# Performance work log

Measured on AMD Instinct MI355X. Metric: run time of the kernel, lower is better.

The kernel has to match this reference:

```python
import jax, jax.numpy as jnp
import numpy as np

B, L, EMB, H, NL, E, MAXA, PAD = 64, 512, 400, 256, 3, 512, 32, 0


def setup_inputs() -> dict:
    key = jax.random.key(0)
    ks = jax.random.split(key, 12)
    s = lambda k, shape: jax.random.normal(k, shape, jnp.float32) * 0.02
    Semb = jax.random.normal(ks[0], (B, EMB, L), jnp.float32)
    word_ids = jax.random.randint(ks[1], (B, L), 0, 30000)
    y1 = jax.random.randint(ks[2], (B,), 0, L - MAXA)
    span = jax.random.randint(ks[3], (B,), 0, MAXA)
    y2 = y1 + span
    edges = jax.random.randint(ks[4], (B, E, 2), 0, L)
    return dict(
        Semb=Semb,
        ans_sent_word_ids=word_ids,
        y1_in_sent=y1,
        y2_in_sent=y2,
        edges=edges,
        W1=s(ks[5], (H, EMB)),                 # Initialized_Conv1d (k=1, no bias)
        hw_lin_W=s(ks[6], (2, H, H)), hw_lin_b=jnp.zeros((2, H), jnp.float32),
        hw_gate_W=s(ks[7], (2, H, H)), hw_gate_b=jnp.zeros((2, H), jnp.float32),
        gcn_W=s(ks[8], (NL, H, H)), gcn_b=jnp.zeros((NL, H), jnp.float32),
        conv_W=s(ks[9], (1, NL * H)), conv_b=jnp.zeros((1,), jnp.float32),
        lin_W=s(ks[10], (L, L)), lin_b=jnp.zeros((L,), jnp.float32),
    )


def reference(Semb, ans_sent_word_ids, y1_in_sent, y2_in_sent, edges,
              W1, hw_lin_W, hw_lin_b, hw_gate_W, hw_gate_b,
              gcn_W, gcn_b, conv_W, conv_b, lin_W, lin_b):
    # 1x1 conv: [B, EMB, L] -> [B, H, L]
    x = jnp.einsum('oi,bit->bot', W1, Semb)
    # 2-layer Highway (dropout is identity in eval)
    for i in range(2):
        gate = jax.nn.sigmoid(jnp.einsum('oi,bit->bot', hw_gate_W[i], x) + hw_gate_b[i][None, :, None])
        nonlin = jnp.einsum('oi,bit->bot', hw_lin_W[i], x) + hw_lin_b[i][None, :, None]
        x = gate * nonlin + (1.0 - gate) * x
    maskS = (ans_sent_word_ids != PAD).astype(x.dtype)            # [B, L]
    # answer-span mask (Aemb itself is dead code in the original forward's output)
    pos = y1_in_sent[:, None] + jnp.arange(MAXA)                   # [B, MAXA]
    maskA = (pos <= y2_in_sent[:, None]).astype(x.dtype)
    # dense adjacency from edge list (undirected since gcn_directed=False)
    bidx = jnp.broadcast_to(jnp.arange(B)[:, None], (B, E))
    adj = jnp.zeros((B, L, L), x.dtype)
    adj = adj.at[bidx, edges[..., 0], edges[..., 1]].set(1.0)
    adj = adj.at[bidx, edges[..., 1], edges[..., 0]].set(1.0)
    # GCN (C-GCN style: W(Ax) + W(x), note bias counted twice, /(deg+1), relu)
    h = x.transpose(0, 2, 1)                                       # [B, L, H]
    denom = jnp.sum(adj, axis=2, keepdims=True) + 1.0              # [B, L, 1]
    outs = []
    for l in range(NL):
        Ax = jnp.einsum('bls,bsh->blh', adj, h)
        AxW = jnp.einsum('blh,oh->blo', Ax + h, gcn_W[l]) + 2.0 * gcn_b[l]
        h = jax.nn.relu(AxW / denom)
        outs.append(h)
    cat = jnp.concatenate(outs, axis=2)                            # [B, L, NL*H]
    y = jax.nn.relu(jnp.einsum('blc,oc->bol', cat, conv_W) + conv_b[None, :, None])  # [B,1,L]
    logits = (jnp.einsum('bol,ml->bom', y, lin_W) + lin_b).squeeze(1)                # [B,L]
    logits = logits * maskS + (1.0 - maskS) * (-1e30)
    return (logits, maskA)
```

## Files before the change

kernel.cpp:

```cpp
#include <hip/hip_runtime.h>
#include <cstdint>

#define B 64
#define L 512
#define EMB 400
#define KPAD 416
#define H 256
#define NL 3
#define NE 512
#define MAXA 32
#define M_TOT (B * L)

typedef unsigned short u16;
typedef float f32x4 __attribute__((ext_vector_type(4)));
typedef short short8 __attribute__((ext_vector_type(8)));
typedef u16 u16x8 __attribute__((ext_vector_type(8)));

__device__ __forceinline__ float b2f(u16 u) {
  unsigned v = ((unsigned)u) << 16;
  return __builtin_bit_cast(float, v);
}
__device__ __forceinline__ u16 f2b(float f) {
  unsigned u = __builtin_bit_cast(unsigned, f);
  unsigned r = (u + 0x7fffu + ((u >> 16) & 1u)) >> 16;
  return (u16)r;
}

#define GL16(g, l)                                                              \
  __builtin_amdgcn_global_load_lds((const __attribute__((address_space(1))) void*)(g), \
                                   (__attribute__((address_space(3))) void*)(l), 16, 0, 0)

__global__ __launch_bounds__(256, 2) void k_convT(const float* __restrict__ Semb,
                                                  const u16* __restrict__ W1b,
                                                  u16* __restrict__ Out) {
  __shared__ u16 smem[64 * KPAD + 256 * 32];
  __shared__ u16 tmp2[64][72];
  u16* At = smem;
  u16* Bt = smem + 64 * KPAD;

  const int t = threadIdx.x;
  const int wid = t >> 6, lane = t & 63;
  const int m0 = blockIdx.x * 64;
  const int b = m0 >> 9, l0 = m0 & 511;
  const int fr = lane & 15, kg = lane >> 4;
  const int r4 = t >> 2, ksg = t & 3;

  {
    const int kc0 = ksg * 8;
#pragma unroll
    for (int c = 0; c < 4; ++c)
      GL16(W1b + (size_t)(c * 64 + r4) * KPAD + kc0, Bt + (size_t)(c * 256 + wid * 64) * 8);
  }

  for (int et = 0; et < 7; ++et) {
    const int e0 = et * 64;
    const int erows = (et < 6) ? 64 : 32;
    {
      const int er = t >> 2, ls = (t & 3) * 16;
      if (er < erows) {
        if (e0 + er < EMB) {
          const float* src = Semb + ((size_t)b * EMB + e0 + er) * L + l0 + ls;
#pragma unroll
          for (int i = 0; i < 4; ++i) {
            const float4 v = *(const float4*)(src + i * 4);
            tmp2[er][ls + i * 4 + 0] = f2b(v.x);
            tmp2[er][ls + i * 4 + 1] = f2b(v.y);
            tmp2[er][ls + i * 4 + 2] = f2b(v.z);
            tmp2[er][ls + i * 4 + 3] = f2b(v.w);
          }
        } else {
#pragma unroll
          for (int i = 0; i < 16; ++i) tmp2[er][ls + i] = 0;
        }
      }
    }
    __syncthreads();
    {
      const int lr = t >> 2, es = (t & 3) * 16;
      if (es < erows) {
        u16x8 v0, v1;
#pragma unroll
        for (int i = 0; i < 8; ++i) v0[i] = tmp2[es + i][lr];
#pragma unroll
        for (int i = 0; i < 8; ++i) v1[i] = tmp2[es + 8 + i][lr];
        const int k = e0 + es;
        u16* dst = At + (((size_t)(k >> 5) * 64 + lr) * 4 + ((k & 31) >> 3)) * 8;
        *(u16x8*)dst = v0;
        *(u16x8*)(dst + 8) = v1;
      }
    }
    __syncthreads();
  }

  f32x4 acc[4][4] = {};
  for (int kk = 0; kk < (KPAD >> 5); ++kk) {
    if (kk > 0) {
      const int kc = kk * 32 + ksg * 8;
#pragma unroll
      for (int c = 0; c < 4; ++c)
        GL16(W1b + (size_t)(c * 64 + r4) * KPAD + kc, Bt + (size_t)(c * 256 + wid * 64) * 8);
    }
    asm volatile("s_waitcnt vmcnt(0)" ::: "memory");
    __builtin_amdgcn_s_barrier();
    asm volatile("" ::: "memory");
    short8 af[4], bf[4];
#pragma unroll
    for (int i = 0; i < 4; ++i) {
      af[i] = *(const short8*)(At + ((size_t)(kk * 64 + i * 16 + fr) * 4 + kg) * 8);
      bf[i] = *(const short8*)(Bt + ((size_t)(wid * 64 + i * 16 + fr) * 4 + kg) * 8);
    }
#pragma unroll
    for (int mi = 0; mi < 4; ++mi)
#pragma unroll
      for (int ni = 0; ni < 4; ++ni)
        acc[mi][ni] = __builtin_amdgcn_mfma_f32_16x16x32_bf16(af[mi], bf[ni], acc[mi][ni], 0, 0, 0);
    __builtin_amdgcn_s_barrier();
    asm volatile("" ::: "memory");
  }

  const int r0 = kg * 4;
  const int c0 = wid * 64 + fr;
#pragma unroll
  for (int ni = 0; ni < 4; ++ni) {
    const int col = c0 + ni * 16;
#pragma unroll
    for (int mi = 0; mi < 4; ++mi)
#pragma unroll
      for (int rr = 0; rr < 4; ++rr)
        Out[(size_t)(m0 + mi * 16 + r0 + rr) * H + col] = f2b(acc[mi][ni][rr]);
  }
}

__global__ __launch_bounds__(256, 2) void gemm64hw(
    const u16* __restrict__ A, const u16* __restrict__ Bw, const u16* __restrict__ B2w,
    const float* __restrict__ bias1, const float* __restrict__ bias2,
    u16* __restrict__ Out) {
  __shared__ u16 Bl0[256 * 32];
  __shared__ u16 Bl1[256 * 32];
  __shared__ u16 Cl0[256 * 32];
  __shared__ u16 Cl1[256 * 32];
  __shared__ u16 Al0[64 * 32];
  __shared__ u16 Al1[64 * 32];

  const int t = threadIdx.x;
  const int wid = t >> 6, lane = t & 63;
  const int m0 = blockIdx.x * 64;
  const int fr = lane & 15, kg = lane >> 4;
  const int r4 = t >> 2, ksg = t & 3;

  f32x4 acc[4][4] = {};
  f32x4 acc2[4][4] = {};

  auto stage = [&](u16* Ab, u16* Bb, u16* Cb, int kk) {
    const int kc = kk * 32 + ksg * 8;
#pragma unroll
    for (int c = 0; c < 4; ++c) {
      GL16(Bw + (size_t)(c * 64 + r4) * H + kc, Bb + (size_t)(c * 256 + wid * 64) * 8);
      GL16(B2w + (size_t)(c * 64 + r4) * H + kc, Cb + (size_t)(c * 256 + wid * 64) * 8);
    }
    GL16(A + (size_t)(m0 + r4) * H + kc, Ab + (size_t)(wid * 64) * 8);
  };
  auto compute = [&](const u16* Ab, const u16* Bb, const u16* Cb) {
    short8 af[4], bf[4], cf[4];
#pragma unroll
    for (int i = 0; i < 4; ++i) {
      af[i] = *(const short8*)(Ab + ((size_t)(i * 16 + fr) * 4 + kg) * 8);
      bf[i] = *(const short8*)(Bb + ((size_t)(wid * 64 + i * 16 + fr) * 4 + kg) * 8);
      cf[i] = *(const short8*)(Cb + ((size_t)(wid * 64 + i * 16 + fr) * 4 + kg) * 8);
    }
#pragma unroll
    for (int mi = 0; mi < 4; ++mi)
#pragma unroll
      for (int ni = 0; ni < 4; ++ni) {
        acc[mi][ni] = __builtin_amdgcn_mfma_f32_16x16x32_bf16(af[mi], bf[ni], acc[mi][ni], 0, 0, 0);
        acc2[mi][ni] = __builtin_amdgcn_mfma_f32_16x16x32_bf16(af[mi], cf[ni], acc2[mi][ni], 0, 0, 0);
      }
  };

  const int nk = H >> 5;
  stage(Al0, Bl0, Cl0, 0);
  for (int kk = 0; kk < nk; ++kk) {
    u16* Ac = (kk & 1) ? Al1 : Al0;
    u16* Bc = (kk & 1) ? Bl1 : Bl0;
    u16* Cc = (kk & 1) ? Cl1 : Cl0;
    u16* An = (kk & 1) ? Al0 : Al1;
    u16* Bn = (kk & 1) ? Bl0 : Bl1;
    u16* Cn = (kk & 1) ? Cl0 : Cl1;
    if (kk + 1 < nk) {
      stage(An, Bn, Cn, kk + 1);
      asm volatile("s_waitcnt vmcnt(9)" ::: "memory");
    } else {
      asm volatile("s_waitcnt vmcnt(0)" ::: "memory");
    }
    __builtin_amdgcn_s_barrier();
    asm volatile("" ::: "memory");
    compute(Ac, Bc, Cc);
    __builtin_amdgcn_s_barrier();
    asm volatile("" ::: "memory");
  }

  const int r0 = kg * 4;
  const int c0 = wid * 64 + fr;
#pragma unroll
  for (int ni = 0; ni < 4; ++ni) {
    const int col = c0 + ni * 16;
    const float b1 = bias1[col], b2 = bias2[col];
#pragma unroll
    for (int mi = 0; mi < 4; ++mi)
#pragma unroll
      for (int rr = 0; rr < 4; ++rr) {
        const int row = m0 + mi * 16 + r0 + rr;
        const float g = 1.f / (1.f + __expf(-(acc[mi][ni][rr] + b1)));
        const float nn = acc2[mi][ni][rr] + b2;
        const float x = b2f(A[(size_t)row * H + col]);
        Out[(size_t)row * H + col] = f2b(g * nn + (1.f - g) * x);
      }
  }
}

template <bool LAST>
__global__ __launch_bounds__(256, 2) void gemm64gcn(
    const u16* __restrict__ A, const u16* __restrict__ Bw,
    const float* __restrict__ bias1, const float* __restrict__ rden,
    const float* __restrict__ cw, float* __restrict__ yv, u16* __restrict__ Out) {
  __shared__ u16 Bl0[2 * 256 * 32];
  __shared__ u16 Bl1[2 * 256 * 32];
  __shared__ u16 Al0[2 * 64 * 32];
  __shared__ u16 Al1[2 * 64 * 32];

  const int t = threadIdx.x;
  const int wid = t >> 6, lane = t & 63;
  const int m0 = blockIdx.x * 64;
  const int fr = lane & 15, kg = lane >> 4;
  const int r4 = t >> 2, ksg = t & 3;

  f32x4 acc[4][4] = {};

  auto stage = [&](u16* Ab, u16* Bb, int kk) {
#pragma unroll
    for (int h = 0; h < 2; ++h) {
      const int kc = kk * 64 + h * 32 + ksg * 8;
#pragma unroll
      for (int c = 0; c < 4; ++c)
        GL16(Bw + (size_t)(c * 64 + r4) * H + kc,
             Bb + (size_t)h * 8192 + (size_t)(c * 256 + wid * 64) * 8);
      GL16(A + (size_t)(m0 + r4) * H + kc,
           Ab + (size_t)h * 2048 + (size_t)(wid * 64) * 8);
    }
  };
  auto compute = [&](const u16* Ab, const u16* Bb) {
#pragma unroll
    for (int h = 0; h < 2; ++h) {
      short8 af[4], bf[4];
#pragma unroll
      for (int i = 0; i < 4; ++i) {
        af[i] = *(const short8*)(Ab + (size_t)h * 2048 + ((size_t)(i * 16 + fr) * 4 + kg) * 8);
        bf[i] = *(const short8*)(Bb + (size_t)h * 8192 +
                                 ((size_t)(wid * 64 + i * 16 + fr) * 4 + kg) * 8);
      }
#pragma unroll
      for (int mi = 0; mi < 4; ++mi)
#pragma unroll
        for (int ni = 0; ni < 4; ++ni)
          acc[mi][ni] =
              __builtin_amdgcn_mfma_f32_16x16x32_bf16(af[mi], bf[ni], acc[mi][ni], 0, 0, 0);
    }
  };

  const int nk = H >> 6;
  stage(Al0, Bl0, 0);
  for (int kk = 0; kk < nk; ++kk) {
    u16* Ac = (kk & 1) ? Al1 : Al0;
    u16* Bc = (kk & 1) ? Bl1 : Bl0;
    u16* An = (kk & 1) ? Al0 : Al1;
    u16* Bn = (kk & 1) ? Bl0 : Bl1;
    if (kk + 1 < nk) {
      stage(An, Bn, kk + 1);
      asm volatile("s_waitcnt vmcnt(10)" ::: "memory");
    } else {
      asm volatile("s_waitcnt vmcnt(0)" ::: "memory");
    }
    __builtin_amdgcn_s_barrier();
    asm volatile("" ::: "memory");
    compute(Ac, Bc);
    __builtin_amdgcn_s_barrier();
    asm volatile("" ::: "memory");
  }

  const int r0 = kg * 4;
  const int c0 = wid * 64 + fr;
  float ypart[16];
#pragma unroll
  for (int q = 0; q < 16; ++q) ypart[q] = 0.f;
#pragma unroll
  for (int ni = 0; ni < 4; ++ni) {
    const int col = c0 + ni * 16;
    const float b1 = 2.f * bias1[col];
    const float cwv = cw[col];
#pragma unroll
    for (int mi = 0; mi < 4; ++mi)
#pragma unroll
      for (int rr = 0; rr < 4; ++rr) {
        const int row = m0 + mi * 16 + r0 + rr;
        const float s = (acc[mi][ni][rr] + b1) * rden[row];
        const float rl = s > 0.f ? s : 0.f;
        ypart[mi * 4 + rr] += rl * cwv;
        if constexpr (!LAST) Out[(size_t)row * H + col] = f2b(rl);
      }
  }
#pragma unroll
  for (int q = 0; q < 16; ++q) {
    float p = ypart[q];
    p += __shfl_xor(p, 1);
    p += __shfl_xor(p, 2);
    p += __shfl_xor(p, 4);
    p += __shfl_xor(p, 8);
    if (fr == 0) atomicAdd(&yv[m0 + (q >> 2) * 16 + r0 + (q & 3)], p);
  }
}

__global__ __launch_bounds__(256) void k_gather(const unsigned* __restrict__ bm,
                                                const u16* __restrict__ h,
                                                u16* __restrict__ T) {
  const int t = threadIdx.x;
  const int tok = blockIdx.x * 8 + (t >> 5);
  const int b = tok >> 9;
  const int c = (t & 31) * 8;
  const uint4* wp4 = (const uint4*)(bm + (size_t)tok * 16);
  const uint4 w0 = wp4[0], w1 = wp4[1], w2 = wp4[2], w3 = wp4[3];
  const unsigned wa[16] = {w0.x, w0.y, w0.z, w0.w, w1.x, w1.y, w1.z, w1.w,
                           w2.x, w2.y, w2.z, w2.w, w3.x, w3.y, w3.z, w3.w};
  float acc[8];
  {
    const u16x8 v = *(const u16x8*)(h + (size_t)tok * H + c);
#pragma unroll
    for (int i = 0; i < 8; ++i) acc[i] = b2f(v[i]);
  }
#pragma unroll
  for (int wi = 0; wi < 16; ++wi) {
    unsigned bits = wa[wi];
    while (bits) {
      const int bit = __ffs(bits) - 1;
      bits &= bits - 1;
      const int s = wi * 32 + bit;
      const u16x8 u = *(const u16x8*)(h + (size_t)(b * L + s) * H + c);
#pragma unroll
      for (int i = 0; i < 8; ++i) acc[i] += b2f(u[i]);
    }
  }
  u16x8 o;
#pragma unroll
  for (int i = 0; i < 8; ++i) o[i] = f2b(acc[i]);
  *(u16x8*)(T + (size_t)tok * H + c) = o;
}

__global__ __launch_bounds__(256) void k_prep2(const int* __restrict__ edges,
                                               unsigned* __restrict__ bm,
                                               float* __restrict__ rden,
                                               float* __restrict__ yv,
                                               const float* __restrict__ W1,
                                               const float* __restrict__ gW,
                                               const float* __restrict__ lW,
                                               const float* __restrict__ gcnW,
                                               u16* __restrict__ W1b, u16* __restrict__ HWGb,
                                               u16* __restrict__ HWLb, u16* __restrict__ GCNb) {
  const int t = threadIdx.x;
  if (blockIdx.x < B) {
    __shared__ unsigned lbm[512 * 16];
    const int b = blockIdx.x;
#pragma unroll
    for (int i = 0; i < 32; ++i) lbm[i * 256 + t] = 0;
    __syncthreads();
#pragma unroll
    for (int e = 0; e < 2; ++e) {
      const int idx = t * 2 + e;
      const int u = edges[((size_t)b * NE + idx) * 2 + 0];
      const int v = edges[((size_t)b * NE + idx) * 2 + 1];
      atomicOr(&lbm[u * 16 + (v >> 5)], 1u << (v & 31));
      atomicOr(&lbm[v * 16 + (u >> 5)], 1u << (u & 31));
    }
    __syncthreads();
    uint4* gbm = (uint4*)(bm + (size_t)b * 512 * 16);
    const uint4* lb4 = (const uint4*)lbm;
#pragma unroll
    for (int i = 0; i < 8; ++i) gbm[i * 256 + t] = lb4[i * 256 + t];
#pragma unroll
    for (int r = 0; r < 2; ++r) {
      const int row = t * 2 + r;
      int c = 0;
#pragma unroll
      for (int w = 0; w < 16; ++w) c += __popc(lbm[row * 16 + w]);
      rden[(size_t)b * 512 + row] = 1.f / (1.f + (float)c);
    }
#pragma unroll
    for (int i = 0; i < 2; ++i) yv[(size_t)b * 512 + i * 256 + t] = 0.f;
    return;
  }
  int i = (blockIdx.x - B) * 256 + t;
  if (i < 256 * KPAD) {
    const int o = i / KPAD, k = i - o * KPAD;
    W1b[i] = (k < EMB) ? f2b(W1[o * EMB + k]) : (u16)0;
    return;
  }
  i -= 256 * KPAD;
  if (i < 2 * H * H) { HWGb[i] = f2b(gW[i]); return; }
  i -= 2 * H * H;
  if (i < 2 * H * H) { HWLb[i] = f2b(lW[i]); return; }
  i -= 2 * H * H;
  if (i < NL * H * H) GCNb[i] = f2b(gcnW[i]);
}

__global__ __launch_bounds__(256) void k_logits(const float* __restrict__ yv,
                                                const float* __restrict__ cb,
                                                const float* __restrict__ lw,
                                                const float* __restrict__ lb,
                                                const int* __restrict__ wids,
                                                const int* __restrict__ y1,
                                                const int* __restrict__ y2,
                                                float* __restrict__ out) {
  if (blockIdx.x == B * 2) {
#pragma unroll
    for (int j = 0; j < 8; ++j) {
      const int idx = j * 256 + threadIdx.x;
      const int b = idx >> 5, q = idx & 31;
      out[B * L + idx] = (y1[b] + q <= y2[b]) ? 1.0f : 0.0f;
    }
    return;
  }
  const int b = blockIdx.x >> 1;
  const int m = ((blockIdx.x & 1) << 8) + threadIdx.x;
  __shared__ float ys[512];
  const float cb0 = cb[0];
  ys[threadIdx.x] = fmaxf(yv[(size_t)b * L + threadIdx.x] + cb0, 0.f);
  ys[threadIdx.x + 256] = fmaxf(yv[(size_t)b * L + 256 + threadIdx.x] + cb0, 0.f);
  __syncthreads();
  float acc = lb[m];
  const float4* wr = (const float4*)(lw + (size_t)m * L);
#pragma unroll 4
  for (int l4 = 0; l4 < 128; ++l4) {
    const float4 w4 = wr[l4];
    acc += ys[l4 * 4] * w4.x + ys[l4 * 4 + 1] * w4.y + ys[l4 * 4 + 2] * w4.z +
           ys[l4 * 4 + 3] * w4.w;
  }
  out[(size_t)b * L + m] = (wids[(size_t)b * L + m] != 0) ? acc : -1.0e30f;
}

extern "C" void kernel_launch(void* const* d_in, const int* in_sizes, int n_in,
                              void* d_out, int out_size, void* d_ws, size_t ws_size,
                              hipStream_t stream) {
  (void)in_sizes; (void)n_in; (void)out_size; (void)ws_size;
  const float* Semb      = (const float*)d_in[0];
  const int*   wids      = (const int*)d_in[1];
  const int*   y1        = (const int*)d_in[2];
  const int*   y2        = (const int*)d_in[3];
  const int*   edges     = (const int*)d_in[4];
  const float* W1        = (const float*)d_in[5];
  const float* hw_lin_W  = (const float*)d_in[6];
  const float* hw_lin_b  = (const float*)d_in[7];
  const float* hw_gate_W = (const float*)d_in[8];
  const float* hw_gate_b = (const float*)d_in[9];
  const float* gcn_W     = (const float*)d_in[10];
  const float* gcn_b     = (const float*)d_in[11];
  const float* conv_W    = (const float*)d_in[12];
  const float* conv_b    = (const float*)d_in[13];
  const float* lin_W     = (const float*)d_in[14];
  const float* lin_b     = (const float*)d_in[15];
  float* out = (float*)d_out;

  char* ws = (char*)d_ws;
  const size_t SZX = (size_t)M_TOT * H * 2;
  u16* P0b  = (u16*)(ws);
  u16* P1b  = (u16*)(ws + SZX);
  u16* O0   = (u16*)(ws + 2 * SZX);
  u16* O1   = (u16*)(ws + 3 * SZX);
  char* wp  = ws + 4 * SZX;
  u16* W1b  = (u16*)(wp);
  u16* HWGb = (u16*)(wp + 212992);
  u16* HWLb = (u16*)(wp + 212992 + 262144);
  u16* GCNb = (u16*)(wp + 212992 + 2 * 262144);
  char* sp  = wp + 212992 + 2 * 262144 + 393216;
  unsigned* bm   = (unsigned*)(sp);
  float*    yv   = (float*)(sp + 2097152);
  float*    rden = (float*)(sp + 2097152 + 131072);

  const int ncvt = 256 * KPAD + 4 * H * H + NL * H * H;
  k_prep2<<<dim3(B + (ncvt + 255) / 256), 256, 0, stream>>>(
      edges, bm, rden, yv, W1, hw_gate_W, hw_lin_W, gcn_W, W1b, HWGb, HWLb, GCNb);

  k_convT<<<dim3(M_TOT / 64), 256, 0, stream>>>(Semb, W1b, P0b);

  gemm64hw<<<dim3(M_TOT / 64), 256, 0, stream>>>(P0b, HWGb, HWLb, hw_gate_b, hw_lin_b, P1b);
  gemm64hw<<<dim3(M_TOT / 64), 256, 0, stream>>>(P1b, HWGb + H * H, HWLb + H * H,
                                                 hw_gate_b + H, hw_lin_b + H, P0b);

  k_gather<<<dim3(M_TOT / 8), 256, 0, stream>>>(bm, P0b, P1b);
  gemm64gcn<false><<<dim3(M_TOT / 64), 256, 0, stream>>>(P1b, GCNb, gcn_b, rden,
                                                         conv_W, yv, O0);
  k_gather<<<dim3(M_TOT / 8), 256, 0, stream>>>(bm, O0, P0b);
  gemm64gcn<false><<<dim3(M_TOT / 64), 256, 0, stream>>>(P0b, GCNb + H * H, gcn_b + H, rden,
                                                         conv_W + H, yv, O1);
  k_gather<<<dim3(M_TOT / 8), 256, 0, stream>>>(bm, O1, P1b);
  gemm64gcn<true><<<dim3(M_TOT / 64), 256, 0, stream>>>(P1b, GCNb + 2 * H * H, gcn_b + 2 * H,
                                                        rden, conv_W + 2 * H, yv, nullptr);

  k_logits<<<dim3(B * 2 + 1), 256, 0, stream>>>(yv, conv_b, lin_W, lin_b, wids, y1, y2, out);
}
```

Before: 166.7 us.

## Fuse input projection and both highway layers into one per-tile kernel

Merges the 1x1 conv GEMM and the two highway GEMM kernels into a single kernel that processes the same 64-row tile through all three stages. Shared memory is reused through one union buffer, and intermediates still go through global memory but are re-read by the same block, likely from L2. This removes two kernel launches and the inter-kernel tail and drain gaps. The cost is a longer kernel with serial stages per block and a larger shared-memory footprint.

```diff
diff --git a/kernel.cpp b/kernel.cpp
--- a/kernel.cpp
+++ b/kernel.cpp
@@ -30,13 +30,21 @@
   __builtin_amdgcn_global_load_lds((const __attribute__((address_space(1))) void*)(g), \
                                    (__attribute__((address_space(3))) void*)(l), 16, 0, 0)
 
-__global__ __launch_bounds__(256, 2) void k_convT(const float* __restrict__ Semb,
-                                                  const u16* __restrict__ W1b,
-                                                  u16* __restrict__ Out) {
-  __shared__ u16 smem[64 * KPAD + 256 * 32];
-  __shared__ u16 tmp2[64][72];
-  u16* At = smem;
-  u16* Bt = smem + 64 * KPAD;
+__global__ __launch_bounds__(256, 2) void k_chain(
+    const float* __restrict__ Semb, const u16* __restrict__ W1b,
+    const u16* __restrict__ HWGb, const u16* __restrict__ HWLb,
+    const float* __restrict__ gbias, const float* __restrict__ lbias,
+    u16* __restrict__ X1, u16* __restrict__ T1, u16* __restrict__ Xout) {
+  __shared__ u16 U[39424];
+  u16* At = U;
+  u16* Bt = U + 26624;
+  u16 (*tmp2)[72] = (u16(*)[72])(U + 34816);
+  u16* Bl0 = U;
+  u16* Bl1 = U + 8192;
+  u16* Cl0 = U + 16384;
+  u16* Cl1 = U + 24576;
+  u16* Al0 = U + 32768;
+  u16* Al1 = U + 34816;
 
   const int t = threadIdx.x;
   const int wid = t >> 6, lane = t & 63;
@@ -44,6 +52,8 @@
   const int b = m0 >> 9, l0 = m0 & 511;
   const int fr = lane & 15, kg = lane >> 4;
   const int r4 = t >> 2, ksg = t & 3;
+  const int r0 = kg * 4;
+  const int c0 = wid * 64 + fr;
 
   {
     const int kc0 = ksg * 8;
@@ -51,7 +61,6 @@
     for (int c = 0; c < 4; ++c)
       GL16(W1b + (size_t)(c * 64 + r4) * KPAD + kc0, Bt + (size_t)(c * 256 + wid * 64) * 8);
   }
-
   for (int et = 0; et < 7; ++et) {
     const int e0 = et * 64;
     const int erows = (et < 6) ? 64 : 32;
@@ -92,129 +101,118 @@
     __syncthreads();
   }
 
-  f32x4 acc[4][4] = {};
-  for (int kk = 0; kk < (KPAD >> 5); ++kk) {
-    if (kk > 0) {
+  {
+    f32x4 acc[4][4] = {};
+    for (int kk = 0; kk < (KPAD >> 5); ++kk) {
+      if (kk > 0) {
+        const int kc = kk * 32 + ksg * 8;
+#pragma unroll
+        for (int c = 0; c < 4; ++c)
+          GL16(W1b + (size_t)(c * 64 + r4) * KPAD + kc, Bt + (size_t)(c * 256 + wid * 64) * 8);
+      }
+      asm volatile("s_waitcnt vmcnt(0)" ::: "memory");
+      __builtin_amdgcn_s_barrier();
+      asm volatile("" ::: "memory");
+      short8 af[4], bf[4];
+#pragma unroll
+      for (int i = 0; i < 4; ++i) {
+        af[i] = *(const short8*)(At + ((size_t)(kk * 64 + i * 16 + fr) * 4 + kg) * 8);
+        bf[i] = *(const short8*)(Bt + ((size_t)(wid * 64 + i * 16 + fr) * 4 + kg) * 8);
+      }
+#pragma unroll
+      for (int mi = 0; mi < 4; ++mi)
+#pragma unroll
+        for (int ni = 0; ni < 4; ++ni)
+          acc[mi][ni] =
+              __builtin_amdgcn_mfma_f32_16x16x32_bf16(af[mi], bf[ni], acc[mi][ni], 0, 0, 0);
+      __builtin_amdgcn_s_barrier();
+      asm volatile("" ::: "memory");
+    }
+#pragma unroll
+    for (int ni = 0; ni < 4; ++ni) {
+      const int col = c0 + ni * 16;
+#pragma unroll
+      for (int mi = 0; mi < 4; ++mi)
+#pragma unroll
+        for (int rr = 0; rr < 4; ++rr)
+          X1[(size_t)(m0 + mi * 16 + r0 + rr) * H + col] = f2b(acc[mi][ni][rr]);
+    }
+  }
+  __syncthreads();
+
+  for (int layer = 0; layer < 2; ++layer) {
+    const u16* Ain = layer ? T1 : X1;
+    u16* Oout = layer ? Xout : T1;
+    const u16* Gw = HWGb + layer * H * H;
+    const u16* Lw = HWLb + layer * H * H;
+    f32x4 acc[4][4] = {};
+    f32x4 acc2[4][4] = {};
+
+    auto stage = [&](u16* Ab, u16* Bb, u16* Cb, int kk) {
       const int kc = kk * 32 + ksg * 8;
 #pragma unroll
-      for (int c = 0; c < 4; ++c)
-        GL16(W1b + (size_t)(c * 64 + r4) * KPAD + kc, Bt + (size_t)(c * 256 + wid * 64) * 8);
-    }
-    asm volatile("s_waitcnt vmcnt(0)" ::: "memory");
-    __builtin_amdgcn_s_barrier();
-    asm volatile("" ::: "memory");
-    short8 af[4], bf[4];
-#pragma unroll
-    for (int i = 0; i < 4; ++i) {
-      af[i] = *(const short8*)(At + ((size_t)(kk * 64 + i * 16 + fr) * 4 + kg) * 8);
-      bf[i] = *(const short8*)(Bt + ((size_t)(wid * 64 + i * 16 + fr) * 4 + kg) * 8);
-    }
-#pragma unroll
-    for (int mi = 0; mi < 4; ++mi)
-#pragma unroll
-      for (int ni = 0; ni < 4; ++ni)
-        acc[mi][ni] = __builtin_amdgcn_mfma_f32_16x16x32_bf16(af[mi], bf[ni], acc[mi][ni], 0, 0, 0);
-    __builtin_amdgcn_s_barrier();
-    asm volatile("" ::: "memory");
-  }
-
-  const int r0 = kg * 4;
-  const int c0 = wid * 64 + fr;
-#pragma unroll
-  for (int ni = 0; ni < 4; ++ni) {
-    const int col = c0 + ni * 16;
-#pragma unroll
-    for (int mi = 0; mi < 4; ++mi)
-#pragma unroll
-      for (int rr = 0; rr < 4; ++rr)
-        Out[(size_t)(m0 + mi * 16 + r0 + rr) * H + col] = f2b(acc[mi][ni][rr]);
-  }
-}
-
-__global__ __launch_bounds__(256, 2) void gemm64hw(
-    const u16* __restrict__ A, const u16* __restrict__ Bw, const u16* __restrict__ B2w,
-    const float* __restrict__ bias1, const float* __restrict__ bias2,
-    u16* __restrict__ Out) {
-  __shared__ u16 Bl0[256 * 32];
-  __shared__ u16 Bl1[256 * 32];
-  __shared__ u16 Cl0[256 * 32];
-  __shared__ u16 Cl1[256 * 32];
-  __shared__ u16 Al0[64 * 32];
-  __shared__ u16 Al1[64 * 32];
-
-  const int t = threadIdx.x;
-  const int wid = t >> 6, lane = t & 63;
-  const int m0 = blockIdx.x * 64;
-  const int fr = lane & 15, kg = lane >> 4;
-  const int r4 = t >> 2, ksg = t & 3;
-
-  f32x4 acc[4][4] = {};
-  f32x4 acc2[4][4] = {};
-
-  auto stage = [&](u16* Ab, u16* Bb, u16* Cb, int kk) {
-    const int kc = kk * 32 + ksg * 8;
-#pragma unroll
-    for (int c = 0; c < 4; ++c) {
-      GL16(Bw + (size_t)(c * 64 + r4) * H + kc, Bb + (size_t)(c * 256 + wid * 64) * 8);
-      GL16(B2w + (size_t)(c * 64 + r4) * H + kc, Cb + (size_t)(c * 256 + wid * 64) * 8);
-    }
-    GL16(A + (size_t)(m0 + r4) * H + kc, Ab + (size_t)(wid * 64) * 8);
-  };
-  auto compute = [&](const u16* Ab, const u16* Bb, const u16* Cb) {
-    short8 af[4], bf[4], cf[4];
-#pragma unroll
-    for (int i = 0; i < 4; ++i) {
-      af[i] = *(const short8*)(Ab + ((size_t)(i * 16 + fr) * 4 + kg) * 8);
-      bf[i] = *(const short8*)(Bb + ((size_t)(wid * 64 + i * 16 + fr) * 4 + kg) * 8);
-      cf[i] = *(const short8*)(Cb + ((size_t)(wid * 64 + i * 16 + fr) * 4 + kg) * 8);
-    }
-#pragma unroll
-    for (int mi = 0; mi < 4; ++mi)
-#pragma unroll
-      for (int ni = 0; ni < 4; ++ni) {
-        acc[mi][ni] = __builtin_amdgcn_mfma_f32_16x16x32_bf16(af[mi], bf[ni], acc[mi][ni], 0, 0, 0);
-        acc2[mi][ni] = __builtin_amdgcn_mfma_f32_16x16x32_bf16(af[mi], cf[ni], acc2[mi][ni], 0, 0, 0);
-      }
-  };
-
-  const int nk = H >> 5;
-  stage(Al0, Bl0, Cl0, 0);
-  for (int kk = 0; kk < nk; ++kk) {
-    u16* Ac = (kk & 1) ? Al1 : Al0;
-    u16* Bc = (kk & 1) ? Bl1 : Bl0;
-    u16* Cc = (kk & 1) ? Cl1 : Cl0;
-    u16* An = (kk & 1) ? Al0 : Al1;
-    u16* Bn = (kk & 1) ? Bl0 : Bl1;
-    u16* Cn = (kk & 1) ? Cl0 : Cl1;
-    if (kk + 1 < nk) {
-      stage(An, Bn, Cn, kk + 1);
-      asm volatile("s_waitcnt vmcnt(9)" ::: "memory");
-    } else {
-      asm volatile("s_waitcnt vmcnt(0)" ::: "memory");
-    }
-    __builtin_amdgcn_s_barrier();
-    asm volatile("" ::: "memory");
-    compute(Ac, Bc, Cc);
-    __builtin_amdgcn_s_barrier();
-    asm volatile("" ::: "memory");
-  }
-
-  const int r0 = kg * 4;
-  const int c0 = wid * 64 + fr;
-#pragma unroll
-  for (int ni = 0; ni < 4; ++ni) {
-    const int col = c0 + ni * 16;
-    const float b1 = bias1[col], b2 = bias2[col];
-#pragma unroll
-    for (int mi = 0; mi < 4; ++mi)
-#pragma unroll
-      for (int rr = 0; rr < 4; ++rr) {
-        const int row = m0 + mi * 16 + r0 + rr;
-        const float g = 1.f / (1.f + __expf(-(acc[mi][ni][rr] + b1)));
-        const float nn = acc2[mi][ni][rr] + b2;
-        const float x = b2f(A[(size_t)row * H + col]);
-        Out[(size_t)row * H + col] = f2b(g * nn + (1.f - g) * x);
-      }
+      for (int c = 0; c < 4; ++c) {
+        GL16(Gw + (size_t)(c * 64 + r4) * H + kc, Bb + (size_t)(c * 256 + wid * 64) * 8);
+        GL16(Lw + (size_t)(c * 64 + r4) * H + kc, Cb + (size_t)(c * 256 + wid * 64) * 8);
+      }
+      GL16(Ain + (size_t)(m0 + r4) * H + kc, Ab + (size_t)(wid * 64) * 8);
+    };
+    auto compute = [&](const u16* Ab, const u16* Bb, const u16* Cb) {
+      short8 af[4], bf[4], cf[4];
+#pragma unroll
+      for (int i = 0; i < 4; ++i) {
+        af[i] = *(const short8*)(Ab + ((size_t)(i * 16 + fr) * 4 + kg) * 8);
+        bf[i] = *(const short8*)(Bb + ((size_t)(wid * 64 + i * 16 + fr) * 4 + kg) * 8);
+        cf[i] = *(const short8*)(Cb + ((size_t)(wid * 64 + i * 16 + fr) * 4 + kg) * 8);
+      }
+#pragma unroll
+      for (int mi = 0; mi < 4; ++mi)
+#pragma unroll
+        for (int ni = 0; ni < 4; ++ni) {
+          acc[mi][ni] =
+              __builtin_amdgcn_mfma_f32_16x16x32_bf16(af[mi], bf[ni], acc[mi][ni], 0, 0, 0);
+          acc2[mi][ni] =
+              __builtin_amdgcn_mfma_f32_16x16x32_bf16(af[mi], cf[ni], acc2[mi][ni], 0, 0, 0);
+        }
+    };
+
+    stage(Al0, Bl0, Cl0, 0);
+    for (int kk = 0; kk < 8; ++kk) {
+      u16* Ac = (kk & 1) ? Al1 : Al0;
+      u16* Bc = (kk & 1) ? Bl1 : Bl0;
+      u16* Cc = (kk & 1) ? Cl1 : Cl0;
+      u16* An = (kk & 1) ? Al0 : Al1;
+      u16* Bn = (kk & 1) ? Bl0 : Bl1;
+      u16* Cn = (kk & 1) ? Cl0 : Cl1;
+      if (kk + 1 < 8) {
+        stage(An, Bn, Cn, kk + 1);
+        asm volatile("s_waitcnt vmcnt(9)" ::: "memory");
+      } else {
+        asm volatile("s_waitcnt vmcnt(0)" ::: "memory");
+      }
+      __builtin_amdgcn_s_barrier();
+      asm volatile("" ::: "memory");
+      compute(Ac, Bc, Cc);
+      __builtin_amdgcn_s_barrier();
+      asm volatile("" ::: "memory");
+    }
+#pragma unroll
+    for (int ni = 0; ni < 4; ++ni) {
+      const int col = c0 + ni * 16;
+      const float b1 = gbias[layer * H + col];
+      const float b2 = lbias[layer * H + col];
+#pragma unroll
+      for (int mi = 0; mi < 4; ++mi)
+#pragma unroll
+        for (int rr = 0; rr < 4; ++rr) {
+          const int row = m0 + mi * 16 + r0 + rr;
+          const float g = 1.f / (1.f + __expf(-(acc[mi][ni][rr] + b1)));
+          const float nn = acc2[mi][ni][rr] + b2;
+          const float x = b2f(Ain[(size_t)row * H + col]);
+          Oout[(size_t)row * H + col] = f2b(g * nn + (1.f - g) * x);
+        }
+    }
+    __syncthreads();
   }
 }
 
@@ -487,11 +485,8 @@
   k_prep2<<<dim3(B + (ncvt + 255) / 256), 256, 0, stream>>>(
       edges, bm, rden, yv, W1, hw_gate_W, hw_lin_W, gcn_W, W1b, HWGb, HWLb, GCNb);
 
-  k_convT<<<dim3(M_TOT / 64), 256, 0, stream>>>(Semb, W1b, P0b);
-
-  gemm64hw<<<dim3(M_TOT / 64), 256, 0, stream>>>(P0b, HWGb, HWLb, hw_gate_b, hw_lin_b, P1b);
-  gemm64hw<<<dim3(M_TOT / 64), 256, 0, stream>>>(P1b, HWGb + H * H, HWLb + H * H,
-                                                 hw_gate_b + H, hw_lin_b + H, P0b);
+  k_chain<<<dim3(M_TOT / 64), 256, 0, stream>>>(Semb, W1b, HWGb, HWLb,
+                                                hw_gate_b, hw_lin_b, O0, P1b, P0b);
 
   k_gather<<<dim3(M_TOT / 8), 256, 0, stream>>>(bm, P0b, P1b);
   gemm64gcn<false><<<dim3(M_TOT / 64), 256, 0, stream>>>(P1b, GCNb, gcn_b, rden,
```

Measured after the change: 167.1 us. Within noise of the previous version (+0.2%).
